# Performance work log

Measured on AMD Instinct MI355X. Metric: run time of the kernel, lower is better.

Reference implementation:

```python
import jax, jax.numpy as jnp
import numpy as np

B, R, D = 16, 2048, 512
H2, NREL = 2 * D, 2048  # relation_mlp hidden = 2*d_model, output = n_relations
MIN_PROB = 0.1          # early-stop probability threshold from the torch code


def setup_inputs() -> dict:
    key = jax.random.key(0)
    ks = jax.random.split(key, 8)
    sc = lambda k, shp: jax.random.normal(k, shp, jnp.float32) * 0.02
    return {
        "rel_encoding": jax.random.normal(ks[0], (B, R, D), jnp.float32),
        "na_emb": jax.random.normal(ks[1], (D,), jnp.float32),
        "v_w": sc(ks[2], (D, D)), "v_b": jnp.zeros((D,), jnp.float32),
        "o_w": sc(ks[3], (D, D)), "o_b": jnp.zeros((D,), jnp.float32),
        "ln_g": jnp.ones((D,), jnp.float32), "ln_b": jnp.zeros((D,), jnp.float32),
        "w1": sc(ks[4], (H2, D)), "b1": jnp.zeros((H2,), jnp.float32),
        "w2": sc(ks[5], (NREL, H2)), "b2": jnp.zeros((NREL,), jnp.float32),
    }


def _ln(x, g, b, eps=1e-5):
    m = jnp.mean(x, axis=-1, keepdims=True)
    v = jnp.var(x, axis=-1, keepdims=True)
    return (x - m) * jax.lax.rsqrt(v + eps) * g + b


def reference(rel_encoding, na_emb, v_w, v_b, o_w, o_b, ln_g, ln_b, w1, b1, w2, b2):
    # Cross-attention with a single key/value token: softmax over a length-1 axis
    # is identically 1, so attn_out = out_proj(v_proj(kv)) for every query position.
    x = rel_encoding                                         # [B,R,D]
    attn = (x @ v_w.T + v_b) @ o_w.T + o_b                   # [B,R,D]

    def step_logits(state):                                  # state broadcasts to [B,R,D]
        h = _ln(attn + state, ln_g, ln_b)                    # residual + layernorm
        return jax.nn.relu(h @ w1.T + b1) @ w2.T + b2        # [B,R,NREL]

    # step 0: query is the na_embedding
    p0 = jax.nn.softmax(step_logits(na_emb), axis=-1)
    m0 = jnp.max(p0, axis=-1)
    i0 = jnp.argmax(p0, axis=-1)
    cont0 = (i0 != 0) & (m0 >= MIN_PROB)                     # else break before step 0 emits

    # step 1: last appended state is the relation encoding itself
    p1 = jax.nn.softmax(step_logits(x), axis=-1)
    m1 = jnp.max(p1, axis=-1)
    i1 = jnp.argmax(p1, axis=-1)
    cont1 = cont0 & (i1 != 0) & (m1 >= MIN_PROB)

    # rule_score = prod of accepted step probs; 0.0 if no step accepted
    scores = jnp.where(cont0, jnp.where(cont1, m0 * m1, m0), 0.0)  # [B,R]
    lengths = cont0.astype(jnp.int32) + cont1.astype(jnp.int32)    # ragged rule lengths
    return scores, i0, i1, lengths
```

## Files before the change

### kernel.cpp

```cpp
#include <hip/hip_runtime.h>
#include <math.h>

#define MTOT 32768
#define DD   512
#define HHD  1024
#define NRELN 2048
#define SCA  64.f
#define SCB  1024.f
#define INVS (1.f / 65536.f)
#define CAPR 4096
#define MARGIN 2.0e-3f

typedef _Float16 h8  __attribute__((ext_vector_type(8)));
typedef float    f4  __attribute__((ext_vector_type(4)));
typedef float    f16v __attribute__((ext_vector_type(16)));

__device__ __forceinline__ void fsplit(float x, _Float16& h, _Float16& l) {
  _Float16 t = (_Float16)x;
  h = t;
  l = (_Float16)(x - (float)t);
}

__device__ __forceinline__ void gld16(const _Float16* g, _Float16* l) {
  __builtin_amdgcn_global_load_lds(
      (const __attribute__((address_space(1))) void*)g,
      (__attribute__((address_space(3))) void*)l, 16, 0, 0);
}


__global__ void prep_wvo_split(const float* __restrict__ vw, const float* __restrict__ ow,
                               _Float16* __restrict__ wh, _Float16* __restrict__ wl) {
  int idx = blockIdx.x * 256 + threadIdx.x;
  int k = idx & 511;
  int n = idx >> 9;
  float s = 0.f;
  for (int j = 0; j < DD; ++j) s += ow[n * DD + j] * vw[j * DD + k];
  fsplit(s * SCB, wh[n * DD + k], wl[n * DD + k]);
}

__global__ void prep_cvec(const float* __restrict__ ow, const float* __restrict__ vb,
                          const float* __restrict__ ob, float* __restrict__ c) {
  int i = blockIdx.x * 256 + threadIdx.x;
  if (i < DD) {
    float s = ob[i];
    for (int k = 0; k < DD; ++k) s += ow[i * DD + k] * vb[k];
    c[i] = s;
  }
}

__global__ void prep_w1p_split(const float* __restrict__ w1, const float* __restrict__ g,
                               _Float16* __restrict__ wh, _Float16* __restrict__ wl) {
  int idx = blockIdx.x * 256 + threadIdx.x;
  int k = idx & 511;
  int n = idx >> 9;
  fsplit(w1[n * DD + k] * g[k] * SCB, wh[n * DD + k], wl[n * DD + k]);
}

__global__ void prep_b1p(const float* __restrict__ w1, const float* __restrict__ lnb,
                         const float* __restrict__ b1, float* __restrict__ b1p) {
  int n = blockIdx.x * 256 + threadIdx.x;
  if (n < HHD) {
    float s = b1[n];
    for (int k = 0; k < DD; ++k) s += w1[n * DD + k] * lnb[k];
    b1p[n] = s;
  }
}

__global__ void prep_w2_split(const float* __restrict__ w2,
                              _Float16* __restrict__ wh, _Float16* __restrict__ wl) {
  int idx = blockIdx.x * 256 + threadIdx.x;
  int k = idx & 1023;
  int n = idx >> 10;
  fsplit(w2[n * HHD + k] * SCB, wh[n * HHD + k], wl[n * HHD + k]);
}

__global__ void split_x(const float* __restrict__ src, _Float16* __restrict__ h,
                        _Float16* __restrict__ l) {
  int idx = (blockIdx.x * 256 + threadIdx.x) * 8;
  float4 a = *(const float4*)(src + idx);
  float4 b = *(const float4*)(src + idx + 4);
  float vv[8] = {a.x, a.y, a.z, a.w, b.x, b.y, b.z, b.w};
  _Float16 hh[8], ll[8];
#pragma unroll
  for (int i = 0; i < 8; ++i) fsplit(vv[i] * SCA, hh[i], ll[i]);
  *(h8*)(h + idx) = *(h8*)hh;
  *(h8*)(l + idx) = *(h8*)ll;
}

__global__ void zero_cnt(int* c) { c[blockIdx.x * 256 + threadIdx.x] = 0; }

template <int MODE, int KDIM, int NTOT>
__global__ __launch_bounds__(256) void gemm_split(
    const _Float16* __restrict__ Ah, const _Float16* __restrict__ Al,
    const _Float16* __restrict__ Bh, const _Float16* __restrict__ Bl,
    const float* __restrict__ bias,
    float* __restrict__ outF,
    _Float16* __restrict__ outHh, _Float16* __restrict__ outHl,
    float* __restrict__ pM, float* __restrict__ pI,
    const int* __restrict__ cntp, int pstr) {
  __shared__ __align__(16) _Float16 sA[2][128][32];
  __shared__ __align__(16) _Float16 sB[2][128][32];
  const int t = threadIdx.x;
  const int lane = t & 63;
  const int wv = t >> 6;
  const int wr = wv & 1, wc = wv >> 1;
  const int l31 = lane & 31, half = lane >> 5;
  const int n0 = blockIdx.y << 7;

  const _Float16* gsp = (wv == 0) ? Ah : (wv == 1) ? Al : (wv == 2) ? Bh : Bl;
  _Float16* lbase = (wv == 0) ? &sA[0][0][0] : (wv == 1) ? &sA[1][0][0]
                  : (wv == 2) ? &sB[0][0][0] : &sB[1][0][0];
  const int srow = lane >> 2;
  const int scp = lane & 3;
  const int swzE = ((srow >> 1) & 3) ^ ((srow >> 3) & 1);
  const int swzO = swzE ^ 2;
  const int swz = ((l31 >> 1) ^ (l31 >> 3)) & 3;

  int nmb;
  if constexpr (MODE == 2) {
    int a = *cntp;
    if (a > CAPR) a = CAPR;
    nmb = (a + 127) >> 7;
  } else {
    nmb = gridDim.x;
  }

  for (int mb = blockIdx.x; mb < nmb; mb += gridDim.x) {
    const int m0 = mb << 7;
    const int gb = (wv < 2) ? m0 : n0;
    const _Float16* gA0 = gsp + (size_t)(gb + srow) * KDIM + ((scp ^ swzE) << 3);
    const _Float16* gA1 = gsp + (size_t)(gb + srow) * KDIM + ((scp ^ swzO) << 3);

    f16v acc[2][2] = {};
    for (int k0 = 0; k0 < KDIM; k0 += 32) {
      __syncthreads();
#pragma unroll
      for (int it = 0; it < 8; ++it)
        gld16(((it & 1) ? gA1 : gA0) + (size_t)(it * 16) * KDIM + k0, lbase + it * 512);
      __syncthreads();
#pragma unroll
      for (int ks = 0; ks < 2; ++ks) {
        const int pos = (((ks << 1) + half) ^ swz) << 3;
        h8 af_h[2], af_l[2], bf_h[2], bf_l[2];
#pragma unroll
        for (int i = 0; i < 2; ++i) {
          const int mr = wr * 64 + i * 32 + l31;
          af_h[i] = *(const h8*)&sA[0][mr][pos];
          af_l[i] = *(const h8*)&sA[1][mr][pos];
        }
#pragma unroll
        for (int j = 0; j < 2; ++j) {
          const int nr = wc * 64 + j * 32 + l31;
          bf_h[j] = *(const h8*)&sB[0][nr][pos];
          bf_l[j] = *(const h8*)&sB[1][nr][pos];
        }
#pragma unroll
        for (int j = 0; j < 2; ++j)
#pragma unroll
          for (int i = 0; i < 2; ++i) {
            acc[i][j] = __builtin_amdgcn_mfma_f32_32x32x16_f16(af_h[i], bf_h[j], acc[i][j], 0, 0, 0);
            acc[i][j] = __builtin_amdgcn_mfma_f32_32x32x16_f16(af_h[i], bf_l[j], acc[i][j], 0, 0, 0);
            acc[i][j] = __builtin_amdgcn_mfma_f32_32x32x16_f16(af_l[i], bf_h[j], acc[i][j], 0, 0, 0);
          }
      }
    }

    float bb[2];
    int gc[2];
#pragma unroll
    for (int j = 0; j < 2; ++j) {
      gc[j] = n0 + wc * 64 + j * 32 + l31;
      bb[j] = bias[gc[j]];
    }
    if constexpr (MODE == 0) {
#pragma unroll
      for (int i = 0; i < 2; ++i)
#pragma unroll
        for (int r = 0; r < 16; ++r) {
          const int row = m0 + wr * 64 + i * 32 + (r & 3) + 8 * (r >> 2) + 4 * half;
#pragma unroll
          for (int j = 0; j < 2; ++j)
            outF[(size_t)row * NTOT + gc[j]] = acc[i][j][r] * INVS + bb[j];
        }
    } else if constexpr (MODE == 1) {
#pragma unroll
      for (int i = 0; i < 2; ++i)
#pragma unroll
        for (int r = 0; r < 16; ++r) {
          const int row = m0 + wr * 64 + i * 32 + (r & 3) + 8 * (r >> 2) + 4 * half;
#pragma unroll
          for (int j = 0; j < 2; ++j) {
            float v = fmaxf(acc[i][j][r] * INVS + bb[j], 0.f) * SCA;
            _Float16 hh, ll;
            fsplit(v, hh, ll);
            outHh[(size_t)row * NTOT + gc[j]] = hh;
            outHl[(size_t)row * NTOT + gc[j]] = ll;
          }
        }
    } else {
      const int slot = blockIdx.y * 2 + wc;
#pragma unroll
      for (int i = 0; i < 2; ++i)
#pragma unroll
        for (int r = 0; r < 16; ++r) {
          float v0 = acc[i][0][r] * INVS + bb[0];
          float v1 = acc[i][1][r] * INVS + bb[1];
          float M;
          int I;
          if (v0 >= v1) { M = v0; I = gc[0]; }
          else          { M = v1; I = gc[1]; }
#pragma unroll
          for (int sh = 1; sh <= 16; sh <<= 1) {
            float M2 = __shfl_xor(M, sh);
            int   I2 = __shfl_xor(I, sh);
            if (M2 > M || (M2 == M && I2 < I)) { M = M2; I = I2; }
          }
          if (l31 == 0) {
            const int grow = m0 + wr * 64 + i * 32 + (r & 3) + 8 * (r >> 2) + 4 * half;
            pM[(size_t)slot * pstr + grow] = M;
            pI[(size_t)slot * pstr + grow] = (float)I;
          }
        }
    }
  }
}

__global__ __launch_bounds__(256) void gemm_approx(
    const _Float16* __restrict__ Ah, const _Float16* __restrict__ Bh,
    const float* __restrict__ bias,
    float* __restrict__ pM, float* __restrict__ pM2,
    float* __restrict__ pS, int* __restrict__ pI, int astr) {
  __shared__ __align__(16) _Float16 sAll[8192];
  const int t = threadIdx.x;
  const int lane = t & 63;
  const int wv = t >> 6;
  const int wr = wv & 1, wc = wv >> 1;
  const int q = lane >> 4, l16 = lane & 15;
  const int nb = blockIdx.x * 2 + (blockIdx.y & 1);
  const int mb = blockIdx.y >> 1;
  const int m0 = mb << 7;
  const int n0 = nb << 7;

  const _Float16* src0[4];
#pragma unroll
  for (int it = 0; it < 4; ++it) {
    int p = it * 256 + t;
    int row = (p & 511) >> 2;
    int cp = p & 3;
    int sw = ((row >> 1) ^ (row >> 3)) & 3;
    const _Float16* base = (p < 512) ? (Ah + (size_t)(m0 + row) * HHD)
                                     : (Bh + (size_t)(n0 + row) * HHD);
    src0[it] = base + ((cp ^ sw) << 3);
  }
  _Float16* dstw = sAll + (size_t)(wv * 64) * 8;

  int offA[4], offB[4];
#pragma unroll
  for (int i = 0; i < 4; ++i) {
    int ra = wr * 64 + i * 16 + l16;
    int swa = ((ra >> 1) ^ (ra >> 3)) & 3;
    offA[i] = ra * 32 + ((q ^ swa) << 3);
    int rb = wc * 64 + i * 16 + l16;
    int swb = ((rb >> 1) ^ (rb >> 3)) & 3;
    offB[i] = 4096 + rb * 32 + ((q ^ swb) << 3);
  }

  f4 acc[4][4] = {};
  for (int k0 = 0; k0 < HHD; k0 += 32) {
    __syncthreads();
#pragma unroll
    for (int it = 0; it < 4; ++it)
      gld16(src0[it] + k0, dstw + it * 2048);
    __syncthreads();
    h8 af[4], bf[4];
#pragma unroll
    for (int i = 0; i < 4; ++i) af[i] = *(const h8*)&sAll[offA[i]];
#pragma unroll
    for (int j = 0; j < 4; ++j) bf[j] = *(const h8*)&sAll[offB[j]];
#pragma unroll
    for (int j = 0; j < 4; ++j)
#pragma unroll
      for (int i = 0; i < 4; ++i)
        acc[i][j] = __builtin_amdgcn_mfma_f32_16x16x32_f16(af[i], bf[j], acc[i][j], 0, 0, 0);
  }

  const int slot = nb * 2 + wc;
  float bb[4];
  int gc[4];
#pragma unroll
  for (int j = 0; j < 4; ++j) {
    gc[j] = n0 + wc * 64 + j * 16 + l16;
    bb[j] = bias[gc[j]];
  }
#pragma unroll
  for (int i = 0; i < 4; ++i)
#pragma unroll
    for (int rr = 0; rr < 4; ++rr) {
      float M = acc[i][0][rr] * INVS + bb[0], M2 = -INFINITY, S = 1.f;
      int I = gc[0];
#pragma unroll
      for (int j = 1; j < 4; ++j) {
        float v = acc[i][j][rr] * INVS + bb[j];
        if (v > M || (v == M && gc[j] < I)) {
          S = S * __expf(M - v) + 1.f; M2 = M; M = v; I = gc[j];
        } else {
          S += __expf(v - M); M2 = fmaxf(M2, v);
        }
      }
#pragma unroll
      for (int sh = 1; sh <= 8; sh <<= 1) {
        float Mo = __shfl_xor(M, sh);
        float M2o = __shfl_xor(M2, sh);
        float So = __shfl_xor(S, sh);
        int   Io = __shfl_xor(I, sh);
        if (Mo > M || (Mo == M && Io < I)) {
          S = S * __expf(M - Mo) + So; M2 = fmaxf(M, M2o); M = Mo; I = Io;
        } else {
          S += So * __expf(Mo - M); M2 = fmaxf(M2, Mo);
        }
      }
      if (l16 == 0) {
        const int grow = m0 + wr * 64 + i * 16 + q * 4 + rr;
        pM[(size_t)slot * astr + grow] = M;
        pM2[(size_t)slot * astr + grow] = M2;
        pS[(size_t)slot * astr + grow] = S;
        pI[(size_t)slot * astr + grow] = I;
      }
    }
}

__global__ void flag_k(const float* __restrict__ pM, const float* __restrict__ pM2,
                       const float* __restrict__ pS, const int* __restrict__ pI,
                       int astr, int rows,
                       float* __restrict__ map, int* __restrict__ iap, int row0,
                       int* __restrict__ list, int* __restrict__ cnt) {
  int r = blockIdx.x * 256 + threadIdx.x;
  if (r >= rows) return;
  float M = pM[r], M2 = pM2[r], S = pS[r];
  int I = pI[r];
  for (int s = 1; s < 32; ++s) {
    size_t o = (size_t)s * astr + r;
    float m = pM[o], m2 = pM2[o], ss = pS[o];
    int ii = pI[o];
    if (m > M || (m == M && ii < I)) {
      M2 = fmaxf(M, m2); S = S * __expf(M - m) + ss; M = m; I = ii;
    } else {
      M2 = fmaxf(M2, m); S += ss * __expf(m - M);
    }
  }
  map[row0 + r] = 1.f / S;
  iap[row0 + r] = I;
  if (M - M2 < MARGIN) {
    int c = atomicAdd(cnt, 1);
    if (c < CAPR) list[c] = r;
  }
}

__global__ void gather_k(const _Float16* __restrict__ Hh, const _Float16* __restrict__ Hl,
                         const int* __restrict__ list, const int* __restrict__ cnt,
                         _Float16* __restrict__ Gh, _Float16* __restrict__ Gl) {
  int b = blockIdx.x;
  int active = *cnt;
  if (active > CAPR) active = CAPR;
  if (b >= active) return;
  int r = list[b];
  int t = threadIdx.x;
  *(h8*)(Gh + (size_t)b * HHD + t * 8) = *(const h8*)(Hh + (size_t)r * HHD + t * 8);
  *(h8*)(Gl + (size_t)b * HHD + t * 8) = *(const h8*)(Hl + (size_t)r * HHD + t * 8);
}

__global__ void rescue_merge(const float* __restrict__ pMr, const float* __restrict__ pIr,
                             const int* __restrict__ list, const int* __restrict__ cnt,
                             int* __restrict__ iap, int row0) {
  int c = blockIdx.x * 256 + threadIdx.x;
  int a = *cnt;
  if (a > CAPR) a = CAPR;
  if (c >= a) return;
  float M = pMr[c];
  int I = (int)pIr[c];
  for (int s = 1; s < 32; ++s) {
    size_t o = (size_t)s * CAPR + c;
    float m = pMr[o];
    int i2 = (int)pIr[o];
    if (m > M || (m == M && i2 < I)) { M = m; I = i2; }
  }
  iap[row0 + list[c]] = I;
}

__global__ __launch_bounds__(256) void ln_dual(
    const float* __restrict__ A, const float* __restrict__ X,
    const float* __restrict__ na,
    _Float16* __restrict__ y0h, _Float16* __restrict__ y0l,
    _Float16* __restrict__ y1h, _Float16* __restrict__ y1l) {
  int t = threadIdx.x;
  int lane = t & 63;
  int w = t >> 6;
  int r = blockIdx.x * 4 + w;
  const float* ap = A + (size_t)r * DD + lane * 8;
  const float* xp = X + (size_t)r * DD + lane * 8;
  const float* np = na + lane * 8;
  float v0[8], v1[8];
  float s0 = 0.f, q0 = 0.f, s1 = 0.f, q1 = 0.f;
#pragma unroll
  for (int i = 0; i < 8; ++i) {
    float a = ap[i];
    v0[i] = a + np[i];
    v1[i] = a + xp[i];
    s0 += v0[i]; q0 += v0[i] * v0[i];
    s1 += v1[i]; q1 += v1[i] * v1[i];
  }
#pragma unroll
  for (int m = 1; m <= 32; m <<= 1) {
    s0 += __shfl_xor(s0, m); q0 += __shfl_xor(q0, m);
    s1 += __shfl_xor(s1, m); q1 += __shfl_xor(q1, m);
  }
  float mu0 = s0 * (1.f / DD), mu1 = s1 * (1.f / DD);
  float rs0 = 1.f / sqrtf(q0 * (1.f / DD) - mu0 * mu0 + 1e-5f);
  float rs1 = 1.f / sqrtf(q1 * (1.f / DD) - mu1 * mu1 + 1e-5f);
  _Float16 h0[8], l0[8], h1[8], l1[8];
#pragma unroll
  for (int i = 0; i < 8; ++i) {
    fsplit((v0[i] - mu0) * rs0 * SCA, h0[i], l0[i]);
    fsplit((v1[i] - mu1) * rs1 * SCA, h1[i], l1[i]);
  }
  *(h8*)(y0h + (size_t)r * DD + lane * 8) = *(h8*)h0;
  *(h8*)(y0l + (size_t)r * DD + lane * 8) = *(h8*)l0;
  *(h8*)(y1h + (size_t)r * DD + lane * 8) = *(h8*)h1;
  *(h8*)(y1l + (size_t)r * DD + lane * 8) = *(h8*)l1;
}

__global__ void finalize_k(const float* __restrict__ map0, const int* __restrict__ iap0,
                           const float* __restrict__ map1, const int* __restrict__ iap1,
                           float* __restrict__ out) {
  int r = blockIdx.x * 256 + threadIdx.x;
  float m0v = map0[r], m1v = map1[r];
  int i0v = iap0[r], i1v = iap1[r];
  bool c0 = (i0v != 0) && (m0v >= 0.1f);
  bool c1 = c0 && (i1v != 0) && (m1v >= 0.1f);
  out[r] = c0 ? (c1 ? m0v * m1v : m0v) : 0.f;
  out[MTOT + r] = (float)i0v;
  out[2 * MTOT + r] = (float)i1v;
  out[3 * MTOT + r] = (float)((c0 ? 1 : 0) + (c1 ? 1 : 0));
}

extern "C" void kernel_launch(void* const* d_in, const int* in_sizes, int n_in,
                              void* d_out, int out_size, void* d_ws, size_t ws_size,
                              hipStream_t stream) {
  const float* X   = (const float*)d_in[0];
  const float* na  = (const float*)d_in[1];
  const float* vw  = (const float*)d_in[2];
  const float* vb  = (const float*)d_in[3];
  const float* ow  = (const float*)d_in[4];
  const float* ob  = (const float*)d_in[5];
  const float* lng = (const float*)d_in[6];
  const float* lnb = (const float*)d_in[7];
  const float* w1  = (const float*)d_in[8];
  const float* b1  = (const float*)d_in[9];
  const float* w2  = (const float*)d_in[10];
  const float* b2  = (const float*)d_in[11];
  float* out = (float*)d_out;

  char* p = (char*)d_ws;
  auto alloc = [&](size_t bytes) -> void* {
    void* r = (void*)p;
    p += (bytes + 255) & ~(size_t)255;
    return r;
  };
  _Float16* wvo_h = (_Float16*)alloc(512 * 512 * 2);
  _Float16* wvo_l = (_Float16*)alloc(512 * 512 * 2);
  float*    cvec  = (float*)alloc(512 * 4);
  _Float16* w1p_h = (_Float16*)alloc(1024 * 512 * 2);
  _Float16* w1p_l = (_Float16*)alloc(1024 * 512 * 2);
  float*    b1p   = (float*)alloc(1024 * 4);
  _Float16* w2_h  = (_Float16*)alloc(2048 * 1024 * 2);
  _Float16* w2_l  = (_Float16*)alloc(2048 * 1024 * 2);
  float* map0 = (float*)alloc((size_t)MTOT * 4);
  float* map1 = (float*)alloc((size_t)MTOT * 4);
  int* iap0 = (int*)alloc((size_t)MTOT * 4);
  int* iap1 = (int*)alloc((size_t)MTOT * 4);
  int* list = (int*)alloc(CAPR * 4);
  int* cnt  = (int*)alloc(512 * 4);
  float* pMr = (float*)alloc((size_t)32 * CAPR * 4);
  float* pIr = (float*)alloc((size_t)32 * CAPR * 4);
  _Float16* Gh = (_Float16*)alloc((size_t)CAPR * HHD * 2);
  _Float16* Gl = (_Float16*)alloc((size_t)CAPR * HHD * 2);

  size_t fixed = (size_t)(p - (char*)d_ws);
  size_t reserve = 2u << 20;
  size_t remain = ws_size > fixed + reserve ? ws_size - fixed - reserve : 0;
  int chunk = (int)(remain / 10752);
  chunk &= ~127;
  if (chunk < 128) chunk = 128;
  if (chunk > MTOT) chunk = MTOT;

  _Float16* xs_h = (_Float16*)alloc((size_t)chunk * 512 * 2);
  _Float16* xs_l = (_Float16*)alloc((size_t)chunk * 512 * 2);
  float*    Abuf = (float*)alloc((size_t)chunk * 512 * 4);
  _Float16* y0_h = (_Float16*)alloc((size_t)chunk * 512 * 2);
  _Float16* y0_l = (_Float16*)alloc((size_t)chunk * 512 * 2);
  _Float16* H_h  = (_Float16*)alloc((size_t)chunk * 1024 * 2);
  _Float16* H_l  = (_Float16*)alloc((size_t)chunk * 1024 * 2);
  float* pMa  = (float*)alloc((size_t)32 * chunk * 4);
  float* pM2a = (float*)alloc((size_t)32 * chunk * 4);
  float* pSa  = (float*)alloc((size_t)32 * chunk * 4);
  int*   pIa  = (int*)alloc((size_t)32 * chunk * 4);
  _Float16* y1_h = xs_h;
  _Float16* y1_l = xs_l;

  zero_cnt<<<2, 256, 0, stream>>>(cnt);
  prep_wvo_split<<<1024, 256, 0, stream>>>(vw, ow, wvo_h, wvo_l);
  prep_cvec<<<2, 256, 0, stream>>>(ow, vb, ob, cvec);
  prep_w1p_split<<<2048, 256, 0, stream>>>(w1, lng, w1p_h, w1p_l);
  prep_b1p<<<4, 256, 0, stream>>>(w1, lnb, b1, b1p);
  prep_w2_split<<<8192, 256, 0, stream>>>(w2, w2_h, w2_l);

  int citer = 0;
  for (int row0 = 0; row0 < MTOT; row0 += chunk, ++citer) {
    int rows = (MTOT - row0 < chunk) ? (MTOT - row0) : chunk;
    split_x<<<rows * 512 / 2048, 256, 0, stream>>>(X + (size_t)row0 * 512, xs_h, xs_l);
    gemm_split<0, 512, 512><<<dim3(rows / 128, 4), 256, 0, stream>>>(
        xs_h, xs_l, wvo_h, wvo_l, cvec, Abuf, nullptr, nullptr,
        nullptr, nullptr, nullptr, 0);
    ln_dual<<<rows / 4, 256, 0, stream>>>(Abuf, X + (size_t)row0 * 512, na,
                                          y0_h, y0_l, y1_h, y1_l);
    for (int s = 0; s < 2; ++s) {
      int* cp = cnt + citer * 2 + s;
      gemm_split<1, 512, 1024><<<dim3(rows / 128, 8), 256, 0, stream>>>(
          s == 0 ? y0_h : y1_h, s == 0 ? y0_l : y1_l, w1p_h, w1p_l, b1p,
          nullptr, H_h, H_l, nullptr, nullptr, nullptr, 0);
      gemm_approx<<<dim3(8, (rows / 128) * 2), 256, 0, stream>>>(
          H_h, w2_h, b2, pMa, pM2a, pSa, pIa, chunk);
      flag_k<<<(rows + 255) / 256, 256, 0, stream>>>(
          pMa, pM2a, pSa, pIa, chunk, rows,
          s == 0 ? map0 : map1, s == 0 ? iap0 : iap1, row0, list, cp);
      gather_k<<<CAPR, 128, 0, stream>>>(H_h, H_l, list, cp, Gh, Gl);
      gemm_split<2, 1024, 2048><<<dim3(32, 16), 256, 0, stream>>>(
          Gh, Gl, w2_h, w2_l, b2, nullptr, nullptr, nullptr,
          pMr, pIr, cp, CAPR);
      rescue_merge<<<CAPR / 256, 256, 0, stream>>>(
          pMr, pIr, list, cp, s == 0 ? iap0 : iap1, row0);
    }
  }
  finalize_k<<<MTOT / 256, 256, 0, stream>>>(map0, iap0, map1, iap1, out);
}
```

Before: 1.487 ms.

## Rewrite approx logits GEMM as 256x256 double-buffered pipelined MFMA kernel

Replaces the 128x128 tile, single-buffer approximate w2 GEMM with a 512-thread, 256x256 tile kernel. It uses a 64-wide K step, double-buffered LDS, global-to-LDS prefetch split into phases that interleave with MFMA groups, explicit waitcnt/barrier scheduling and setprio. The goal is to hide global load latency and raise operand reuse in the dominant GEMM. The trade-offs are 128KB of LDS per block, higher register pressure from 32 accumulators per wave, and a chunk size that must now be a multiple of 256. The per-slot reduction layout changes to 4 column slots per block, so 32 slots are still produced.

```diff
diff --git a/kernel.cpp b/kernel.cpp
--- a/kernel.cpp
+++ b/kernel.cpp
@@ -225,84 +225,133 @@
   }
 }
 
-__global__ __launch_bounds__(256) void gemm_approx(
+
+#define SBAR __builtin_amdgcn_s_barrier()
+#define SCHB __builtin_amdgcn_sched_barrier(0)
+#define LW0  asm volatile("s_waitcnt lgkmcnt(0)" ::: "memory")
+#define VW(N) asm volatile("s_waitcnt vmcnt(" #N ")" ::: "memory")
+#define VWNONE ((void)0)
+
+#define GLB(k, ktn, nb_)                                                      \
+  gld16(Bh + (size_t)(sBb + (k) * 16384 + (ktn) * 64),                        \
+        lds + 32768 + dBb + (k) * 1024 + (nb_) * 16384)
+#define GLA(k, ktn, nb_)                                                      \
+  gld16(Ah + (size_t)(sAb + (k) * 32768 + (ktn) * 64),                        \
+        lds + dAb + (k) * 2048 + (nb_) * 16384)
+
+#define PHASE(p, cbuf, STAGE, VWS)                                            \
+  {                                                                           \
+    h8 a00 = *(const h8*)(lds + (cbuf) + aRow + (2 * (p)) * 1024 + kc0);      \
+    h8 a01 = *(const h8*)(lds + (cbuf) + aRow + (2 * (p)) * 1024 + kc1);      \
+    h8 a10 = *(const h8*)(lds + (cbuf) + aRow + (2 * (p) + 1) * 1024 + kc0);  \
+    h8 a11 = *(const h8*)(lds + (cbuf) + aRow + (2 * (p) + 1) * 1024 + kc1);  \
+    STAGE;                                                                    \
+    SBAR;                                                                     \
+    LW0;                                                                      \
+    SCHB;                                                                     \
+    __builtin_amdgcn_s_setprio(1);                                            \
+    _Pragma("unroll") for (int j = 0; j < 4; ++j) {                           \
+      acc[2 * (p)][j] = __builtin_amdgcn_mfma_f32_16x16x32_f16(               \
+          a00, bf0[j], acc[2 * (p)][j], 0, 0, 0);                             \
+      acc[2 * (p)][j] = __builtin_amdgcn_mfma_f32_16x16x32_f16(               \
+          a01, bf1[j], acc[2 * (p)][j], 0, 0, 0);                             \
+      acc[2 * (p) + 1][j] = __builtin_amdgcn_mfma_f32_16x16x32_f16(           \
+          a10, bf0[j], acc[2 * (p) + 1][j], 0, 0, 0);                         \
+      acc[2 * (p) + 1][j] = __builtin_amdgcn_mfma_f32_16x16x32_f16(           \
+          a11, bf1[j], acc[2 * (p) + 1][j], 0, 0, 0);                         \
+    }                                                                         \
+    __builtin_amdgcn_s_setprio(0);                                            \
+    VWS;                                                                      \
+    SBAR;                                                                     \
+  }
+
+__global__ __launch_bounds__(512, 2) void gemm_approx(
     const _Float16* __restrict__ Ah, const _Float16* __restrict__ Bh,
     const float* __restrict__ bias,
     float* __restrict__ pM, float* __restrict__ pM2,
     float* __restrict__ pS, int* __restrict__ pI, int astr) {
-  __shared__ __align__(16) _Float16 sAll[8192];
+  __shared__ __align__(16) _Float16 lds[65536];
   const int t = threadIdx.x;
   const int lane = t & 63;
   const int wv = t >> 6;
-  const int wr = wv & 1, wc = wv >> 1;
-  const int q = lane >> 4, l16 = lane & 15;
-  const int nb = blockIdx.x * 2 + (blockIdx.y & 1);
-  const int mb = blockIdx.y >> 1;
-  const int m0 = mb << 7;
-  const int n0 = nb << 7;
-
-  const _Float16* src0[4];
-#pragma unroll
-  for (int it = 0; it < 4; ++it) {
-    int p = it * 256 + t;
-    int row = (p & 511) >> 2;
-    int cp = p & 3;
-    int sw = ((row >> 1) ^ (row >> 3)) & 3;
-    const _Float16* base = (p < 512) ? (Ah + (size_t)(m0 + row) * HHD)
-                                     : (Bh + (size_t)(n0 + row) * HHD);
-    src0[it] = base + ((cp ^ sw) << 3);
-  }
-  _Float16* dstw = sAll + (size_t)(wv * 64) * 8;
-
-  int offA[4], offB[4];
-#pragma unroll
-  for (int i = 0; i < 4; ++i) {
-    int ra = wr * 64 + i * 16 + l16;
-    int swa = ((ra >> 1) ^ (ra >> 3)) & 3;
-    offA[i] = ra * 32 + ((q ^ swa) << 3);
-    int rb = wc * 64 + i * 16 + l16;
-    int swb = ((rb >> 1) ^ (rb >> 3)) & 3;
-    offB[i] = 4096 + rb * 32 + ((q ^ swb) << 3);
-  }
-
-  f4 acc[4][4] = {};
-  for (int k0 = 0; k0 < HHD; k0 += 32) {
-    __syncthreads();
-#pragma unroll
-    for (int it = 0; it < 4; ++it)
-      gld16(src0[it] + k0, dstw + it * 2048);
-    __syncthreads();
-    h8 af[4], bf[4];
-#pragma unroll
-    for (int i = 0; i < 4; ++i) af[i] = *(const h8*)&sAll[offA[i]];
-#pragma unroll
-    for (int j = 0; j < 4; ++j) bf[j] = *(const h8*)&sAll[offB[j]];
-#pragma unroll
-    for (int j = 0; j < 4; ++j)
-#pragma unroll
-      for (int i = 0; i < 4; ++i)
-        acc[i][j] = __builtin_amdgcn_mfma_f32_16x16x32_f16(af[i], bf[j], acc[i][j], 0, 0, 0);
-  }
-
-  const int slot = nb * 2 + wc;
+  const int wr = wv >> 2;
+  const int wc = wv & 3;
+  const int q = lane >> 4;
+  const int l16 = lane & 15;
+  const int s7 = l16 & 7;
+  const int l8 = lane >> 3;
+  const int lc = lane & 7;
+  const int nb = blockIdx.x;
+  const int mb = blockIdx.y;
+  const int m0 = mb << 8;
+  const int n0 = nb << 8;
+
+  const int swz8 = (lc ^ l8) << 3;
+  const int sBb = (n0 + wc * 64 + wr * 8 + l8) * HHD + swz8;
+  const int dBb = (wc * 64 + wr * 8) * 64;
+  const int sAb = (m0 + wr * 128 + wc * 8 + l8) * HHD + swz8;
+  const int dAb = (wr * 128 + wc * 8) * 64;
+
+  const int kc0 = ((q) ^ s7) << 3;
+  const int kc1 = ((q + 4) ^ s7) << 3;
+  const int aRow = (wr * 128 + l16) * 64;
+  const int bRow = 32768 + (wc * 64 + l16) * 64;
+
+  f4 acc[8][4] = {};
+
+  GLB(0, 0, 0); GLB(1, 0, 0); GLB(2, 0, 0); GLB(3, 0, 0);
+  GLA(0, 0, 0); GLA(1, 0, 0); GLA(2, 0, 0); GLA(3, 0, 0);
+  VW(3);
+  SBAR;
+
+  for (int kt = 0; kt < 15; ++kt) {
+    const int cb = (kt & 1) << 14;
+    const int nbuf = (kt & 1) ^ 1;
+    const int ktn = kt + 1;
+    h8 bf0[4], bf1[4];
+#pragma unroll
+    for (int j = 0; j < 4; ++j) {
+      bf0[j] = *(const h8*)(lds + cb + bRow + j * 1024 + kc0);
+      bf1[j] = *(const h8*)(lds + cb + bRow + j * 1024 + kc1);
+    }
+    PHASE(0, cb, GLB(0, ktn, nbuf); GLB(1, ktn, nbuf), VW(4));
+    PHASE(1, cb, GLB(2, ktn, nbuf); GLB(3, ktn, nbuf), VW(5));
+    PHASE(2, cb, GLA(0, ktn, nbuf); GLA(1, ktn, nbuf), VW(6));
+    PHASE(3, cb, GLA(2, ktn, nbuf); GLA(3, ktn, nbuf), VW(3));
+  }
+  {
+    const int cb = 16384;
+    h8 bf0[4], bf1[4];
+#pragma unroll
+    for (int j = 0; j < 4; ++j) {
+      bf0[j] = *(const h8*)(lds + cb + bRow + j * 1024 + kc0);
+      bf1[j] = *(const h8*)(lds + cb + bRow + j * 1024 + kc1);
+    }
+    PHASE(0, cb, VWNONE, VW(2));
+    PHASE(1, cb, VWNONE, VW(1));
+    PHASE(2, cb, VWNONE, VW(0));
+    PHASE(3, cb, VWNONE, VWNONE);
+  }
+
+  const int slot = nb * 4 + wc;
   float bb[4];
-  int gc[4];
+  int gcx[4];
 #pragma unroll
   for (int j = 0; j < 4; ++j) {
-    gc[j] = n0 + wc * 64 + j * 16 + l16;
-    bb[j] = bias[gc[j]];
-  }
-#pragma unroll
-  for (int i = 0; i < 4; ++i)
+    gcx[j] = n0 + wc * 64 + j * 16 + l16;
+    bb[j] = bias[gcx[j]];
+  }
+#pragma unroll
+  for (int i = 0; i < 8; ++i)
 #pragma unroll
     for (int rr = 0; rr < 4; ++rr) {
       float M = acc[i][0][rr] * INVS + bb[0], M2 = -INFINITY, S = 1.f;
-      int I = gc[0];
+      int I = gcx[0];
 #pragma unroll
       for (int j = 1; j < 4; ++j) {
         float v = acc[i][j][rr] * INVS + bb[j];
-        if (v > M || (v == M && gc[j] < I)) {
-          S = S * __expf(M - v) + 1.f; M2 = M; M = v; I = gc[j];
+        if (v > M || (v == M && gcx[j] < I)) {
+          S = S * __expf(M - v) + 1.f; M2 = M; M = v; I = gcx[j];
         } else {
           S += __expf(v - M); M2 = fmaxf(M2, v);
         }
@@ -320,7 +369,7 @@
         }
       }
       if (l16 == 0) {
-        const int grow = m0 + wr * 64 + i * 16 + q * 4 + rr;
+        const int grow = m0 + wr * 128 + i * 16 + q * 4 + rr;
         pM[(size_t)slot * astr + grow] = M;
         pM2[(size_t)slot * astr + grow] = M2;
         pS[(size_t)slot * astr + grow] = S;
@@ -489,8 +538,8 @@
   size_t reserve = 2u << 20;
   size_t remain = ws_size > fixed + reserve ? ws_size - fixed - reserve : 0;
   int chunk = (int)(remain / 10752);
-  chunk &= ~127;
-  if (chunk < 128) chunk = 128;
+  chunk &= ~255;
+  if (chunk < 256) chunk = 256;
   if (chunk > MTOT) chunk = MTOT;
 
   _Float16* xs_h = (_Float16*)alloc((size_t)chunk * 512 * 2);
@@ -528,7 +577,7 @@
       gemm_split<1, 512, 1024><<<dim3(rows / 128, 8), 256, 0, stream>>>(
           s == 0 ? y0_h : y1_h, s == 0 ? y0_l : y1_l, w1p_h, w1p_l, b1p,
           nullptr, H_h, H_l, nullptr, nullptr, nullptr, 0);
-      gemm_approx<<<dim3(8, (rows / 128) * 2), 256, 0, stream>>>(
+      gemm_approx<<<dim3(8, rows / 256), 512, 0, stream>>>(
           H_h, w2_h, b2, pMa, pM2a, pSa, pIa, chunk);
       flag_k<<<(rows + 255) / 256, 256, 0, stream>>>(
           pMa, pM2a, pSa, pIa, chunk, rows,
```

New measurement: 1.566 ms. 5.3% more time.

## Rework approximate logits GEMM with 32x32 MFMA, K=64 tiles, grouped block swizzle

Applied to the files above, without the earlier changes.

The fp16 approximate H·W2 GEMM now uses 32x32x16 MFMA instructions with a 2x2 accumulator tile per wave, loads 64-wide K slices per iteration with an XOR-swizzled LDS layout, and remaps block IDs into groups of eight M-tiles for L2 reuse of W2. It also raises the wave priority around the MFMA section and adds an occupancy hint to launch bounds. The epilogue reduction is adapted to the 32-lane output layout. The intent is fewer LDS reads and syncs per FLOP and better cache locality. The cost is a doubled LDS footprint and a chunk size rounded to multiples of 256 rows. The tie-break on equal logits was also dropped from the in-thread comparison.

```diff
diff --git a/kernel.cpp b/kernel.cpp
--- a/kernel.cpp
+++ b/kernel.cpp
@@ -225,90 +225,91 @@
   }
 }
 
-__global__ __launch_bounds__(256) void gemm_approx(
+
+__global__ __launch_bounds__(256, 4) void gemm_approx(
     const _Float16* __restrict__ Ah, const _Float16* __restrict__ Bh,
     const float* __restrict__ bias,
     float* __restrict__ pM, float* __restrict__ pM2,
     float* __restrict__ pS, int* __restrict__ pI, int astr) {
-  __shared__ __align__(16) _Float16 sAll[8192];
+  __shared__ __align__(16) _Float16 lds[16384];
   const int t = threadIdx.x;
   const int lane = t & 63;
   const int wv = t >> 6;
-  const int wr = wv & 1, wc = wv >> 1;
-  const int q = lane >> 4, l16 = lane & 15;
-  const int nb = blockIdx.x * 2 + (blockIdx.y & 1);
-  const int mb = blockIdx.y >> 1;
+  const int wr = wv >> 1;
+  const int wc = wv & 1;
+  const int l31 = lane & 31, half = lane >> 5;
+
+  const int Tm = gridDim.y >> 1;
+  const int id = blockIdx.x + (blockIdx.y << 3);
+  const int g8 = (id >> 7) << 3;
+  const int r0 = id & 127;
+  int mb, nb;
+  if (g8 + 8 <= Tm) { mb = g8 + (r0 & 7); nb = r0 >> 3; }
+  else { int rem = Tm - g8; mb = g8 + (r0 % rem); nb = r0 / rem; }
   const int m0 = mb << 7;
   const int n0 = nb << 7;
 
-  const _Float16* src0[4];
-#pragma unroll
-  for (int it = 0; it < 4; ++it) {
-    int p = it * 256 + t;
-    int row = (p & 511) >> 2;
-    int cp = p & 3;
-    int sw = ((row >> 1) ^ (row >> 3)) & 3;
-    const _Float16* base = (p < 512) ? (Ah + (size_t)(m0 + row) * HHD)
-                                     : (Bh + (size_t)(n0 + row) * HHD);
-    src0[it] = base + ((cp ^ sw) << 3);
-  }
-  _Float16* dstw = sAll + (size_t)(wv * 64) * 8;
-
-  int offA[4], offB[4];
-#pragma unroll
-  for (int i = 0; i < 4; ++i) {
-    int ra = wr * 64 + i * 16 + l16;
-    int swa = ((ra >> 1) ^ (ra >> 3)) & 3;
-    offA[i] = ra * 32 + ((q ^ swa) << 3);
-    int rb = wc * 64 + i * 16 + l16;
-    int swb = ((rb >> 1) ^ (rb >> 3)) & 3;
-    offB[i] = 4096 + rb * 32 + ((q ^ swb) << 3);
-  }
-
-  f4 acc[4][4] = {};
-  for (int k0 = 0; k0 < HHD; k0 += 32) {
+  const int srow = t >> 3;
+  const int schk = (t & 7) ^ (srow & 7);
+  const int sAb = (m0 + srow) * HHD + schk * 8;
+  const int sBb = (n0 + srow) * HHD + schk * 8;
+  _Float16* dA = lds + t * 8;
+  _Float16* dB = lds + 8192 + t * 8;
+
+  int aks[4], bks[4];
+#pragma unroll
+  for (int ks = 0; ks < 4; ++ks) {
+    int chk = ((ks << 1) + half) ^ (l31 & 7);
+    aks[ks] = (wr * 64 + l31) * 64 + chk * 8;
+    bks[ks] = 8192 + (wc * 64 + l31) * 64 + chk * 8;
+  }
+
+  f16v acc[2][2] = {};
+
+  for (int kt = 0; kt < 16; ++kt) {
     __syncthreads();
 #pragma unroll
-    for (int it = 0; it < 4; ++it)
-      gld16(src0[it] + k0, dstw + it * 2048);
+    for (int i = 0; i < 4; ++i) {
+      gld16(Ah + (size_t)(sAb + i * 32 * HHD + kt * 64), dA + i * 2048);
+      gld16(Bh + (size_t)(sBb + i * 32 * HHD + kt * 64), dB + i * 2048);
+    }
     __syncthreads();
-    h8 af[4], bf[4];
-#pragma unroll
-    for (int i = 0; i < 4; ++i) af[i] = *(const h8*)&sAll[offA[i]];
-#pragma unroll
-    for (int j = 0; j < 4; ++j) bf[j] = *(const h8*)&sAll[offB[j]];
-#pragma unroll
-    for (int j = 0; j < 4; ++j)
-#pragma unroll
-      for (int i = 0; i < 4; ++i)
-        acc[i][j] = __builtin_amdgcn_mfma_f32_16x16x32_f16(af[i], bf[j], acc[i][j], 0, 0, 0);
+    __builtin_amdgcn_s_setprio(1);
+#pragma unroll
+    for (int ks = 0; ks < 4; ++ks) {
+      h8 af0 = *(const h8*)(lds + aks[ks]);
+      h8 af1 = *(const h8*)(lds + aks[ks] + 2048);
+      h8 bf0 = *(const h8*)(lds + bks[ks]);
+      h8 bf1 = *(const h8*)(lds + bks[ks] + 2048);
+      acc[0][0] = __builtin_amdgcn_mfma_f32_32x32x16_f16(af0, bf0, acc[0][0], 0, 0, 0);
+      acc[0][1] = __builtin_amdgcn_mfma_f32_32x32x16_f16(af0, bf1, acc[0][1], 0, 0, 0);
+      acc[1][0] = __builtin_amdgcn_mfma_f32_32x32x16_f16(af1, bf0, acc[1][0], 0, 0, 0);
+      acc[1][1] = __builtin_amdgcn_mfma_f32_32x32x16_f16(af1, bf1, acc[1][1], 0, 0, 0);
+    }
+    __builtin_amdgcn_s_setprio(0);
   }
 
   const int slot = nb * 2 + wc;
-  float bb[4];
-  int gc[4];
-#pragma unroll
-  for (int j = 0; j < 4; ++j) {
-    gc[j] = n0 + wc * 64 + j * 16 + l16;
-    bb[j] = bias[gc[j]];
-  }
-#pragma unroll
-  for (int i = 0; i < 4; ++i)
-#pragma unroll
-    for (int rr = 0; rr < 4; ++rr) {
+  float bb[2];
+  int gcx[2];
+#pragma unroll
+  for (int j = 0; j < 2; ++j) {
+    gcx[j] = n0 + wc * 64 + j * 32 + l31;
+    bb[j] = bias[gcx[j]];
+  }
+#pragma unroll
+  for (int i = 0; i < 2; ++i)
+#pragma unroll
+    for (int rr = 0; rr < 16; ++rr) {
       float M = acc[i][0][rr] * INVS + bb[0], M2 = -INFINITY, S = 1.f;
-      int I = gc[0];
-#pragma unroll
-      for (int j = 1; j < 4; ++j) {
-        float v = acc[i][j][rr] * INVS + bb[j];
-        if (v > M || (v == M && gc[j] < I)) {
-          S = S * __expf(M - v) + 1.f; M2 = M; M = v; I = gc[j];
-        } else {
-          S += __expf(v - M); M2 = fmaxf(M2, v);
-        }
+      int I = gcx[0];
+      {
+        float v = acc[i][1][rr] * INVS + bb[1];
+        if (v > M) { S = S * __expf(M - v) + 1.f; M2 = M; M = v; I = gcx[1]; }
+        else       { S += __expf(v - M); M2 = fmaxf(M2, v); }
       }
 #pragma unroll
-      for (int sh = 1; sh <= 8; sh <<= 1) {
+      for (int sh = 1; sh <= 16; sh <<= 1) {
         float Mo = __shfl_xor(M, sh);
         float M2o = __shfl_xor(M2, sh);
         float So = __shfl_xor(S, sh);
@@ -319,8 +320,8 @@
           S += So * __expf(Mo - M); M2 = fmaxf(M2, Mo);
         }
       }
-      if (l16 == 0) {
-        const int grow = m0 + wr * 64 + i * 16 + q * 4 + rr;
+      if (l31 == 0) {
+        const int grow = m0 + wr * 64 + i * 32 + (rr & 3) + 8 * (rr >> 2) + 4 * half;
         pM[(size_t)slot * astr + grow] = M;
         pM2[(size_t)slot * astr + grow] = M2;
         pS[(size_t)slot * astr + grow] = S;
@@ -489,8 +490,8 @@
   size_t reserve = 2u << 20;
   size_t remain = ws_size > fixed + reserve ? ws_size - fixed - reserve : 0;
   int chunk = (int)(remain / 10752);
-  chunk &= ~127;
-  if (chunk < 128) chunk = 128;
+  chunk &= ~255;
+  if (chunk < 256) chunk = 256;
   if (chunk > MTOT) chunk = MTOT;
 
   _Float16* xs_h = (_Float16*)alloc((size_t)chunk * 512 * 2);
@@ -528,7 +529,7 @@
       gemm_split<1, 512, 1024><<<dim3(rows / 128, 8), 256, 0, stream>>>(
           s == 0 ? y0_h : y1_h, s == 0 ? y0_l : y1_l, w1p_h, w1p_l, b1p,
           nullptr, H_h, H_l, nullptr, nullptr, nullptr, 0);
-      gemm_approx<<<dim3(8, (rows / 128) * 2), 256, 0, stream>>>(
+      gemm_approx<<<dim3(8, rows / 64), 256, 0, stream>>>(
           H_h, w2_h, b2, pMa, pM2a, pSa, pIa, chunk);
       flag_k<<<(rows + 255) / 256, 256, 0, stream>>>(
           pMa, pM2a, pSa, pIa, chunk, rows,
```

New measurement: 1.588 ms. +6.8%, slower.
